# Kernel tuning notes

Hardware: AMD Instinct MI355X
Metric: run time of the kernel (lower is better)

## Reference

```python
import jax, jax.numpy as jnp
import numpy as np

E = 8      # n_rm_states
D = 256    # flattened input dim
H = 64     # hidden width (hard-coded in module)
A = 18     # n_actions
B = 65536  # batch


def setup_inputs() -> dict:
    key = jax.random.key(0)
    ks = jax.random.split(key, 16)
    s = lambda k, shape, fan_in: jax.random.normal(k, shape, jnp.float32) * (1.0 / np.sqrt(fan_in))
    inp = {
        "state": jax.random.normal(ks[0], (B, D), jnp.float32),
        "rm_state": jax.random.randint(ks[1], (B,), 0, E),
        # stacked per-expert params: layer i weight [E, in, out], bias [E, out]
        "W1": s(ks[2], (E, D, H), D), "b1": jnp.zeros((E, H), jnp.float32),
        "W2": s(ks[3], (E, H, H), H), "b2": jnp.zeros((E, H), jnp.float32),
        "W3": s(ks[4], (E, H, H), H), "b3": jnp.zeros((E, H), jnp.float32),
        "W4": s(ks[5], (E, H, H), H), "b4": jnp.zeros((E, H), jnp.float32),
        "W5": s(ks[6], (E, H, H), H), "b5": jnp.zeros((E, H), jnp.float32),
        "W6": s(ks[7], (E, H, A), H), "b6": jnp.zeros((E, A), jnp.float32),
    }
    return inp


def reference(state, rm_state, W1, b1, W2, b2, W3, b3, W4, b4, W5, b5, W6, b6):
    x = state.reshape(state.shape[0], -1)              # [B, D]
    # Run all E expert MLPs densely over the batch, then select per-row expert.
    h = jax.nn.relu(jnp.einsum('bd,edh->ebh', x, W1) + b1[:, None, :])   # [E, B, H]
    h = jax.nn.relu(jnp.einsum('ebh,ehk->ebk', h, W2) + b2[:, None, :])
    h = jax.nn.relu(jnp.einsum('ebh,ehk->ebk', h, W3) + b3[:, None, :])
    h = jax.nn.relu(jnp.einsum('ebh,ehk->ebk', h, W4) + b4[:, None, :])
    h = jax.nn.relu(jnp.einsum('ebh,ehk->ebk', h, W5) + b5[:, None, :])
    out_all = jnp.einsum('ebh,eha->eba', h, W6) + b6[:, None, :]          # [E, B, A]
    # scatter-back: actions[b] = expert[rm_state[b]](x[b])
    actions = out_all[rm_state, jnp.arange(x.shape[0])]                    # [B, A]
    return actions
```

## Files before the change

kernel.cpp:

```cpp
#include <hip/hip_runtime.h>
#include <hip/hip_bf16.h>


#define NE   8
#define DIM  256
#define HID  64
#define NA   18

typedef __attribute__((ext_vector_type(8))) short short8;
typedef __attribute__((ext_vector_type(4))) float f32x4;
#define MFMA __builtin_amdgcn_mfma_f32_16x16x32_bf16

__device__ __forceinline__ unsigned short f2bf(float f) {
    unsigned u = __builtin_bit_cast(unsigned, f);
    u += 0x7fff + ((u >> 16) & 1);
    return (unsigned short)(u >> 16);
}
__device__ __forceinline__ float bf2f(unsigned short h) {
    unsigned u = ((unsigned)h) << 16;
    return __builtin_bit_cast(float, u);
}
__device__ __forceinline__ void split8v(const float* xs, short8& hi, short8& lo) {
    float back[8];
    #pragma unroll
    for (int p = 0; p < 4; ++p) {
        __hip_bfloat162 h2 = __float22bfloat162_rn(make_float2(xs[2*p], xs[2*p+1]));
        hi[2*p]   = (short)__builtin_bit_cast(unsigned short, h2.x);
        hi[2*p+1] = (short)__builtin_bit_cast(unsigned short, h2.y);
        float2 b2 = __bfloat1622float2(h2);
        back[2*p] = b2.x; back[2*p+1] = b2.y;
    }
    #pragma unroll
    for (int p = 0; p < 4; ++p) {
        __hip_bfloat162 l2 = __float22bfloat162_rn(
            make_float2(xs[2*p] - back[2*p], xs[2*p+1] - back[2*p+1]));
        lo[2*p]   = (short)__builtin_bit_cast(unsigned short, l2.x);
        lo[2*p+1] = (short)__builtin_bit_cast(unsigned short, l2.y);
    }
}

__global__ __launch_bounds__(256) void prep_histo(
    const float* __restrict__ W1, const float* __restrict__ W2,
    const float* __restrict__ W3, const float* __restrict__ W4,
    const float* __restrict__ W5, const float* __restrict__ W6,
    short* __restrict__ W1H, short* __restrict__ W1L,
    short* __restrict__ W2H, short* __restrict__ W2L,
    short* __restrict__ W3H, short* __restrict__ W3L,
    short* __restrict__ W4H, short* __restrict__ W4L,
    short* __restrict__ W5H, short* __restrict__ W5L,
    short* __restrict__ W6H, short* __restrict__ W6L,
    const int* __restrict__ rm, int* __restrict__ hist) {
    const int bid = blockIdx.x;
    if (bid >= 136) {
        __shared__ int wch[4][NE];
        const int blk = bid - 136;
        const int t = threadIdx.x, w = t >> 6, l = t & 63;
        const int e = rm[blk * 256 + t];
        #pragma unroll
        for (int q = 0; q < NE; ++q) {
            unsigned long long m = __ballot(e == q);
            if (l == 0) wch[w][q] = __popcll(m);
        }
        __syncthreads();
        if (t < NE) hist[blk * NE + t] = wch[0][t] + wch[1][t] + wch[2][t] + wch[3][t];
        return;
    }
    const int u = bid * 256 + threadIdx.x;
    const float* src; int sstride, dbase, n, npad;
    short *H, *L;
    if (u < 16384) {
        int e = u >> 11, r = u & 2047;
        int ks = r >> 8, nt = (r >> 6) & 3, l = r & 63;
        int k0 = ks * 32 + ((l >> 4) << 3); n = (nt << 4) + (l & 15);
        src = W1 + ((size_t)(e * DIM + k0)) * HID + n;
        sstride = HID; npad = HID;
        H = W1H; L = W1L; dbase = e * 16384 + ((ks * 4 + nt) * 64 + l) * 8;
    } else if (u < 32768) {
        int u2 = u - 16384;
        int layer = u2 >> 12, local = u2 & 4095;
        int e = local >> 9, r = local & 511;
        int ks = r >> 8, nt = (r >> 6) & 3, l = r & 63;
        int k0 = ks * 32 + ((l >> 4) << 3); n = (nt << 4) + (l & 15);
        const float* W = (layer == 0) ? W2 : (layer == 1) ? W3 : (layer == 2) ? W4 : W5;
        src = W + ((size_t)(e * HID + k0)) * HID + n;
        sstride = HID; npad = HID;
        H = (layer == 0) ? W2H : (layer == 1) ? W3H : (layer == 2) ? W4H : W5H;
        L = (layer == 0) ? W2L : (layer == 1) ? W3L : (layer == 2) ? W4L : W5L;
        dbase = e * 4096 + ((ks * 4 + nt) * 64 + l) * 8;
    } else {
        int u3 = u - 32768;
        int e = u3 >> 8, r = u3 & 255;
        int ks = r >> 7, nt = (r >> 6) & 1, l = r & 63;
        int k0 = ks * 32 + ((l >> 4) << 3); n = (nt << 4) + (l & 15);
        src = W6 + ((size_t)(e * HID + k0)) * NA + n;
        sstride = NA; npad = NA;
        H = W6H; L = W6L; dbase = e * 2048 + ((ks * 2 + nt) * 64 + l) * 8;
    }
    short8 hs, ls;
    #pragma unroll
    for (int j = 0; j < 8; ++j) {
        float v = (n < npad) ? src[j * sstride] : 0.0f;
        unsigned short h = f2bf(v);
        hs[j] = (short)h;
        ls[j] = (short)f2bf(v - bf2f(h));
    }
    *(short8*)(H + dbase) = hs;
    *(short8*)(L + dbase) = ls;
}

__global__ __launch_bounds__(512) void scan_scatter(const int* __restrict__ rm,
                                                    const int* __restrict__ hist,
                                                    int* __restrict__ perm,
                                                    int* __restrict__ meta) {
    __shared__ int sbuf[NE][256];
    __shared__ int wc[8][NE];
    __shared__ int wb2[4][NE];
    __shared__ int baseE[NE];
    const int t = threadIdx.x, w = t >> 6, l = t & 63;
    const int myblk = blockIdx.x;

    {
        int v0 = hist[(l * 4 + 0) * NE + w];
        int v1 = hist[(l * 4 + 1) * NE + w];
        int v2 = hist[(l * 4 + 2) * NE + w];
        int v3 = hist[(l * 4 + 3) * NE + w];
        v1 += v0; v2 += v1; v3 += v2;
        int s = v3;
        #pragma unroll
        for (int off = 1; off < 64; off <<= 1) {
            int u = __shfl_up(s, off);
            if (l >= off) s += u;
        }
        const int ex = s - v3;
        sbuf[w][l * 4 + 0] = ex + v0;
        sbuf[w][l * 4 + 1] = ex + v1;
        sbuf[w][l * 4 + 2] = ex + v2;
        sbuf[w][l * 4 + 3] = ex + v3;
    }
    __syncthreads();
    if (t < NE) {
        int es = 0;
        for (int q = 0; q < t; ++q) es += sbuf[q][255];
        baseE[t] = es + (myblk ? sbuf[t][myblk - 1] : 0);
    }
    if (myblk == 0 && t == 0) {
        int es = 0, ts = 0;
        meta[8] = 0; meta[17] = 0;
        for (int e = 0; e < NE; ++e) {
            int c = sbuf[e][255];
            meta[e] = c;
            es += c; meta[8 + e + 1] = es;
            ts += (c + 127) >> 7; meta[17 + e + 1] = ts;
        }
    }
    const int i = myblk * 256 + t;
    const int e_row = (t < 256) ? rm[i] : -1;
    const unsigned long long ltm = (1ull << l) - 1ull;
    int rank = 0;
    #pragma unroll
    for (int q = 0; q < NE; ++q) {
        unsigned long long m = __ballot(e_row == q);
        if (e_row == q) rank = __popcll(m & ltm);
        if (l == 0) wc[w][q] = __popcll(m);
    }
    __syncthreads();
    if (t < 32) {
        int ww = t >> 3, q = t & 7;
        int b = baseE[q];
        for (int p = 0; p < ww; ++p) b += wc[p][q];
        wb2[ww][q] = b;
    }
    __syncthreads();
    if (t < 256) perm[wb2[w][e_row] + rank] = i;
}

template <int NT>
__device__ __forceinline__ void gemm2_k64(const float* h0, const float* h1, int l,
                                          const short* __restrict__ WH,
                                          const short* __restrict__ WL,
                                          f32x4 (*a0)[NT], f32x4 (*a1)[NT],
                                          f32x4 (*a2)[NT]) {
    const int lg = l >> 4, lr = l & 15;
    #pragma unroll
    for (int ks = 0; ks < 2; ++ks) {
        const float* ap0 = h0 + lr * 68 + ks * 32 + lg * 8;
        const float* ap1 = h1 + lr * 68 + ks * 32 + lg * 8;
        float4 u0 = *(const float4*)(ap0);
        float4 u1 = *(const float4*)(ap0 + 4);
        float4 v0 = *(const float4*)(ap1);
        float4 v1 = *(const float4*)(ap1 + 4);
        float xs0[8] = {u0.x, u0.y, u0.z, u0.w, u1.x, u1.y, u1.z, u1.w};
        float xs1[8] = {v0.x, v0.y, v0.z, v0.w, v1.x, v1.y, v1.z, v1.w};
        short8 ahi0, alo0, ahi1, alo1;
        split8v(xs0, ahi0, alo0);
        split8v(xs1, ahi1, alo1);
        short8 bh[NT], bl[NT];
        #pragma unroll
        for (int nt = 0; nt < NT; ++nt) {
            bh[nt] = *(const short8*)(WH + ((ks * NT + nt) * 64 + l) * 8);
            bl[nt] = *(const short8*)(WL + ((ks * NT + nt) * 64 + l) * 8);
        }
        #pragma unroll
        for (int nt = 0; nt < NT; ++nt) {
            a0[0][nt] = MFMA(ahi0, bh[nt], a0[0][nt], 0, 0, 0);
            a0[1][nt] = MFMA(ahi1, bh[nt], a0[1][nt], 0, 0, 0);
            a1[0][nt] = MFMA(alo0, bh[nt], a1[0][nt], 0, 0, 0);
            a1[1][nt] = MFMA(alo1, bh[nt], a1[1][nt], 0, 0, 0);
            a2[0][nt] = MFMA(ahi0, bl[nt], a2[0][nt], 0, 0, 0);
            a2[1][nt] = MFMA(ahi1, bl[nt], a2[1][nt], 0, 0, 0);
        }
    }
}

template <int NT, bool RELU>
__device__ __forceinline__ void finish2(float* h0, float* h1, int l,
                                        const float* __restrict__ bias,
                                        f32x4 (*a0)[NT], f32x4 (*a1)[NT],
                                        f32x4 (*a2)[NT]) {
    const int lg = l >> 4, lr = l & 15;
    #pragma unroll
    for (int nt = 0; nt < NT; ++nt) {
        float bv = bias[nt * 16 + lr];
        #pragma unroll
        for (int r = 0; r < 4; ++r) {
            float v0 = (a0[0][nt][r] + a1[0][nt][r]) + (a2[0][nt][r] + bv);
            float v1 = (a0[1][nt][r] + a1[1][nt][r]) + (a2[1][nt][r] + bv);
            if (RELU) { v0 = fmaxf(v0, 0.0f); v1 = fmaxf(v1, 0.0f); }
            h0[(lg * 4 + r) * 68 + nt * 16 + lr] = v0;
            h1[(lg * 4 + r) * 68 + nt * 16 + lr] = v1;
        }
    }
}

__global__ __launch_bounds__(256, 2) void mlp_mfma(
    const float* __restrict__ x, const int* __restrict__ perm,
    const int* __restrict__ meta,
    const short* __restrict__ W1H, const short* __restrict__ W1L,
    const short* __restrict__ W2H, const short* __restrict__ W2L,
    const short* __restrict__ W3H, const short* __restrict__ W3L,
    const short* __restrict__ W4H, const short* __restrict__ W4L,
    const short* __restrict__ W5H, const short* __restrict__ W5L,
    const short* __restrict__ W6H, const short* __restrict__ W6L,
    const float* __restrict__ b1, const float* __restrict__ b2,
    const float* __restrict__ b3, const float* __restrict__ b4,
    const float* __restrict__ b5, const float* __restrict__ b6,
    float* __restrict__ out) {
    __shared__ __align__(16) float hbuf[4][2][16][68];
    const int blk = blockIdx.x;
    if (blk >= meta[17 + NE]) return;
    int e = 0;
    #pragma unroll 1
    while (blk >= meta[17 + e + 1]) ++e;
    const int lt = blk - meta[17 + e];
    const int cnt = meta[e];
    const int pbase = meta[8 + e];
    const int t = threadIdx.x, w = t >> 6, l = t & 63;
    const int lg = l >> 4, lr = l & 15;
    const int li0 = lt * 128 + w * 32 + lr;
    const int li1 = li0 + 16;
    const int row0 = perm[pbase + min(li0, cnt - 1)];
    const int row1 = perm[pbase + min(li1, cnt - 1)];
    float* h0 = &hbuf[w][0][0][0];
    float* h1 = &hbuf[w][1][0][0];
    const f32x4 zero = {0.0f, 0.0f, 0.0f, 0.0f};

    {
        f32x4 a0[2][4], a1[2][4], a2[2][4];
        #pragma unroll
        for (int m = 0; m < 2; ++m)
            #pragma unroll
            for (int nt = 0; nt < 4; ++nt) { a0[m][nt] = zero; a1[m][nt] = zero; a2[m][nt] = zero; }
        const float* xr0 = x + (size_t)row0 * DIM + lg * 8;
        const float* xr1 = x + (size_t)row1 * DIM + lg * 8;
        const short* WHp = W1H + (size_t)e * 16384 + l * 8;
        const short* WLp = W1L + (size_t)e * 16384 + l * 8;
        #pragma unroll
        for (int ks = 0; ks < 8; ++ks) {
            float4 u0 = *(const float4*)(xr0 + ks * 32);
            float4 u1 = *(const float4*)(xr0 + ks * 32 + 4);
            float4 v0 = *(const float4*)(xr1 + ks * 32);
            float4 v1 = *(const float4*)(xr1 + ks * 32 + 4);
            float xs0[8] = {u0.x, u0.y, u0.z, u0.w, u1.x, u1.y, u1.z, u1.w};
            float xs1[8] = {v0.x, v0.y, v0.z, v0.w, v1.x, v1.y, v1.z, v1.w};
            short8 ahi0, alo0, ahi1, alo1;
            split8v(xs0, ahi0, alo0);
            split8v(xs1, ahi1, alo1);
            short8 bh[4], bl[4];
            #pragma unroll
            for (int nt = 0; nt < 4; ++nt) {
                bh[nt] = *(const short8*)(WHp + (ks * 4 + nt) * 512);
                bl[nt] = *(const short8*)(WLp + (ks * 4 + nt) * 512);
            }
            #pragma unroll
            for (int nt = 0; nt < 4; ++nt) {
                a0[0][nt] = MFMA(ahi0, bh[nt], a0[0][nt], 0, 0, 0);
                a0[1][nt] = MFMA(ahi1, bh[nt], a0[1][nt], 0, 0, 0);
                a1[0][nt] = MFMA(alo0, bh[nt], a1[0][nt], 0, 0, 0);
                a1[1][nt] = MFMA(alo1, bh[nt], a1[1][nt], 0, 0, 0);
                a2[0][nt] = MFMA(ahi0, bl[nt], a2[0][nt], 0, 0, 0);
                a2[1][nt] = MFMA(ahi1, bl[nt], a2[1][nt], 0, 0, 0);
            }
        }
        finish2<4, true>(h0, h1, l, b1 + e * HID, a0, a1, a2);
    }
    #define HIDDEN(WH_, WL_, bias_)                                         \
    {                                                                       \
        f32x4 a0[2][4], a1[2][4], a2[2][4];                                 \
        _Pragma("unroll")                                                   \
        for (int m = 0; m < 2; ++m)                                         \
            _Pragma("unroll")                                               \
            for (int nt = 0; nt < 4; ++nt) { a0[m][nt] = zero; a1[m][nt] = zero; a2[m][nt] = zero; } \
        gemm2_k64<4>(h0, h1, l, WH_ + e * 4096, WL_ + e * 4096, a0, a1, a2);\
        finish2<4, true>(h0, h1, l, bias_ + e * HID, a0, a1, a2);           \
    }
    HIDDEN(W2H, W2L, b2)
    HIDDEN(W3H, W3L, b3)
    HIDDEN(W4H, W4L, b4)
    HIDDEN(W5H, W5L, b5)
    #undef HIDDEN
    {
        f32x4 a0[2][2], a1[2][2], a2[2][2];
        #pragma unroll
        for (int m = 0; m < 2; ++m)
            #pragma unroll
            for (int nt = 0; nt < 2; ++nt) { a0[m][nt] = zero; a1[m][nt] = zero; a2[m][nt] = zero; }
        gemm2_k64<2>(h0, h1, l, W6H + e * 2048, W6L + e * 2048, a0, a1, a2);
        const float* b6p = b6 + e * NA;
        #pragma unroll
        for (int m = 0; m < 2; ++m) {
            const int rowm = m ? row1 : row0;
            #pragma unroll
            for (int r = 0; r < 4; ++r) {
                const int drow = lg * 4 + r;
                const int rs = __shfl(rowm, drow, 64);
                const bool valid = (lt * 128 + w * 32 + m * 16 + drow) < cnt;
                #pragma unroll
                for (int nt = 0; nt < 2; ++nt) {
                    const int col = nt * 16 + lr;
                    if (valid && col < NA)
                        out[(size_t)rs * NA + col] =
                            (a0[m][nt][r] + a1[m][nt][r]) + (a2[m][nt][r] + b6p[col]);
                }
            }
        }
    }
}

extern "C" void kernel_launch(void* const* d_in, const int* in_sizes, int n_in,
                              void* d_out, int out_size, void* d_ws, size_t ws_size,
                              hipStream_t stream) {
    const float* x  = (const float*)d_in[0];
    const int*   rm = (const int*)d_in[1];
    const float* W1 = (const float*)d_in[2];   const float* b1 = (const float*)d_in[3];
    const float* W2 = (const float*)d_in[4];   const float* b2 = (const float*)d_in[5];
    const float* W3 = (const float*)d_in[6];   const float* b3 = (const float*)d_in[7];
    const float* W4 = (const float*)d_in[8];   const float* b4 = (const float*)d_in[9];
    const float* W5 = (const float*)d_in[10];  const float* b5 = (const float*)d_in[11];
    const float* W6 = (const float*)d_in[12];  const float* b6 = (const float*)d_in[13];
    float* out = (float*)d_out;

    const int B = in_sizes[1];
    const int nblk = B / 256;

    int* hist = (int*)d_ws;
    int* meta = hist + nblk * NE;
    int* perm = meta + 32;
    short* W1H = (short*)(perm + B);
    short* W1L = W1H + 131072;
    short* W2H = W1L + 131072;  short* W2L = W2H + 32768;
    short* W3H = W2L + 32768;   short* W3L = W3H + 32768;
    short* W4H = W3L + 32768;   short* W4L = W4H + 32768;
    short* W5H = W4L + 32768;   short* W5L = W5H + 32768;
    short* W6H = W5L + 32768;   short* W6L = W6H + 16384;

    prep_histo<<<136 + nblk, 256, 0, stream>>>(W1, W2, W3, W4, W5, W6,
                                               W1H, W1L, W2H, W2L, W3H, W3L,
                                               W4H, W4L, W5H, W5L, W6H, W6L,
                                               rm, hist);
    scan_scatter<<<nblk, 512, 0, stream>>>(rm, hist, perm, meta);
    mlp_mfma<<<B / 128 + NE, 256, 0, stream>>>(x, perm, meta,
                                               W1H, W1L, W2H, W2L, W3H, W3L,
                                               W4H, W4L, W5H, W5L, W6H, W6L,
                                               b1, b2, b3, b4, b5, b6, out);
}
```

Baseline: 155.2 us.

## Split K across waves with 32-row tiles and shared-memory partial sum reduction

Each block now handles 32 rows instead of 128. Its four waves split the work as 2 row groups times 2 K halves, and each wave writes a partial sum to shared memory. The next layer adds the two partials and applies ReLU while loading them. Launch bounds rise to allow 8 blocks per CU, and the grid is four times larger. The intent is more parallelism and occupancy per expert tile and less padding waste per expert, at the cost of extra __syncthreads per layer, fewer row-tiles to reuse each weight load across, and a serialized scalar epilogue.

```diff
diff --git a/kernel.cpp b/kernel.cpp
--- a/kernel.cpp
+++ b/kernel.cpp
@@ -150,7 +150,7 @@
             int c = sbuf[e][255];
             meta[e] = c;
             es += c; meta[8 + e + 1] = es;
-            ts += (c + 127) >> 7; meta[17 + e + 1] = ts;
+            ts += (c + 31) >> 5; meta[17 + e + 1] = ts;
         }
     }
     const int i = myblk * 256 + t;
@@ -174,65 +174,50 @@
     if (t < 256) perm[wb2[w][e_row] + rank] = i;
 }
 
+__device__ __forceinline__ void read_split(const float* pa, const float* pb, int off,
+                                           short8& hi, short8& lo) {
+    float4 a0 = *(const float4*)(pa + off);
+    float4 a1 = *(const float4*)(pa + off + 4);
+    float4 b0 = *(const float4*)(pb + off);
+    float4 b1 = *(const float4*)(pb + off + 4);
+    float xs[8] = {fmaxf(a0.x + b0.x, 0.0f), fmaxf(a0.y + b0.y, 0.0f),
+                   fmaxf(a0.z + b0.z, 0.0f), fmaxf(a0.w + b0.w, 0.0f),
+                   fmaxf(a1.x + b1.x, 0.0f), fmaxf(a1.y + b1.y, 0.0f),
+                   fmaxf(a1.z + b1.z, 0.0f), fmaxf(a1.w + b1.w, 0.0f)};
+    split8v(xs, hi, lo);
+}
+
 template <int NT>
-__device__ __forceinline__ void gemm2_k64(const float* h0, const float* h1, int l,
-                                          const short* __restrict__ WH,
-                                          const short* __restrict__ WL,
-                                          f32x4 (*a0)[NT], f32x4 (*a1)[NT],
-                                          f32x4 (*a2)[NT]) {
+__device__ __forceinline__ void mfma_slice(const short* __restrict__ WH,
+                                           const short* __restrict__ WL,
+                                           int l, int kh,
+                                           const short8& ahi, const short8& alo,
+                                           f32x4* acc) {
+    #pragma unroll
+    for (int nt = 0; nt < NT; ++nt) {
+        short8 bh = *(const short8*)(WH + (kh * NT + nt) * 512 + l * 8);
+        short8 bl = *(const short8*)(WL + (kh * NT + nt) * 512 + l * 8);
+        acc[nt] = MFMA(ahi, bh, acc[nt], 0, 0, 0);
+        acc[nt] = MFMA(alo, bh, acc[nt], 0, 0, 0);
+        acc[nt] = MFMA(ahi, bl, acc[nt], 0, 0, 0);
+    }
+}
+
+template <int NT>
+__device__ __forceinline__ void write_partial(float* pw, int l,
+                                              const float* __restrict__ bias,
+                                              const f32x4* acc) {
     const int lg = l >> 4, lr = l & 15;
     #pragma unroll
-    for (int ks = 0; ks < 2; ++ks) {
-        const float* ap0 = h0 + lr * 68 + ks * 32 + lg * 8;
-        const float* ap1 = h1 + lr * 68 + ks * 32 + lg * 8;
-        float4 u0 = *(const float4*)(ap0);
-        float4 u1 = *(const float4*)(ap0 + 4);
-        float4 v0 = *(const float4*)(ap1);
-        float4 v1 = *(const float4*)(ap1 + 4);
-        float xs0[8] = {u0.x, u0.y, u0.z, u0.w, u1.x, u1.y, u1.z, u1.w};
-        float xs1[8] = {v0.x, v0.y, v0.z, v0.w, v1.x, v1.y, v1.z, v1.w};
-        short8 ahi0, alo0, ahi1, alo1;
-        split8v(xs0, ahi0, alo0);
-        split8v(xs1, ahi1, alo1);
-        short8 bh[NT], bl[NT];
-        #pragma unroll
-        for (int nt = 0; nt < NT; ++nt) {
-            bh[nt] = *(const short8*)(WH + ((ks * NT + nt) * 64 + l) * 8);
-            bl[nt] = *(const short8*)(WL + ((ks * NT + nt) * 64 + l) * 8);
-        }
-        #pragma unroll
-        for (int nt = 0; nt < NT; ++nt) {
-            a0[0][nt] = MFMA(ahi0, bh[nt], a0[0][nt], 0, 0, 0);
-            a0[1][nt] = MFMA(ahi1, bh[nt], a0[1][nt], 0, 0, 0);
-            a1[0][nt] = MFMA(alo0, bh[nt], a1[0][nt], 0, 0, 0);
-            a1[1][nt] = MFMA(alo1, bh[nt], a1[1][nt], 0, 0, 0);
-            a2[0][nt] = MFMA(ahi0, bl[nt], a2[0][nt], 0, 0, 0);
-            a2[1][nt] = MFMA(ahi1, bl[nt], a2[1][nt], 0, 0, 0);
-        }
-    }
-}
-
-template <int NT, bool RELU>
-__device__ __forceinline__ void finish2(float* h0, float* h1, int l,
-                                        const float* __restrict__ bias,
-                                        f32x4 (*a0)[NT], f32x4 (*a1)[NT],
-                                        f32x4 (*a2)[NT]) {
-    const int lg = l >> 4, lr = l & 15;
-    #pragma unroll
     for (int nt = 0; nt < NT; ++nt) {
-        float bv = bias[nt * 16 + lr];
-        #pragma unroll
-        for (int r = 0; r < 4; ++r) {
-            float v0 = (a0[0][nt][r] + a1[0][nt][r]) + (a2[0][nt][r] + bv);
-            float v1 = (a0[1][nt][r] + a1[1][nt][r]) + (a2[1][nt][r] + bv);
-            if (RELU) { v0 = fmaxf(v0, 0.0f); v1 = fmaxf(v1, 0.0f); }
-            h0[(lg * 4 + r) * 68 + nt * 16 + lr] = v0;
-            h1[(lg * 4 + r) * 68 + nt * 16 + lr] = v1;
-        }
-    }
-}
-
-__global__ __launch_bounds__(256, 2) void mlp_mfma(
+        float bv = bias ? bias[nt * 16 + lr] : 0.0f;
+        #pragma unroll
+        for (int r = 0; r < 4; ++r)
+            pw[(lg * 4 + r) * 68 + nt * 16 + lr] = acc[nt][r] + bv;
+    }
+}
+
+__global__ __launch_bounds__(256, 8) void mlp_mfma(
     const float* __restrict__ x, const int* __restrict__ perm,
     const int* __restrict__ meta,
     const short* __restrict__ W1H, const short* __restrict__ W1L,
@@ -245,7 +230,7 @@
     const float* __restrict__ b3, const float* __restrict__ b4,
     const float* __restrict__ b5, const float* __restrict__ b6,
     float* __restrict__ out) {
-    __shared__ __align__(16) float hbuf[4][2][16][68];
+    __shared__ __align__(16) float hbuf[2][2][16][68];
     const int blk = blockIdx.x;
     if (blk >= meta[17 + NE]) return;
     int e = 0;
@@ -255,93 +240,82 @@
     const int cnt = meta[e];
     const int pbase = meta[8 + e];
     const int t = threadIdx.x, w = t >> 6, l = t & 63;
+    const int m = w >> 1, kh = w & 1;
     const int lg = l >> 4, lr = l & 15;
-    const int li0 = lt * 128 + w * 32 + lr;
-    const int li1 = li0 + 16;
-    const int row0 = perm[pbase + min(li0, cnt - 1)];
-    const int row1 = perm[pbase + min(li1, cnt - 1)];
-    float* h0 = &hbuf[w][0][0][0];
-    float* h1 = &hbuf[w][1][0][0];
+    const int li = lt * 32 + m * 16 + lr;
+    const int row = perm[pbase + min(li, cnt - 1)];
+
+    float* pw = &hbuf[kh][m][0][0];
+    const float* pa = &hbuf[0][m][0][0];
+    const float* pb = &hbuf[1][m][0][0];
+    const int roff = lr * 68 + kh * 32 + lg * 8;
     const f32x4 zero = {0.0f, 0.0f, 0.0f, 0.0f};
 
     {
-        f32x4 a0[2][4], a1[2][4], a2[2][4];
-        #pragma unroll
-        for (int m = 0; m < 2; ++m)
-            #pragma unroll
-            for (int nt = 0; nt < 4; ++nt) { a0[m][nt] = zero; a1[m][nt] = zero; a2[m][nt] = zero; }
-        const float* xr0 = x + (size_t)row0 * DIM + lg * 8;
-        const float* xr1 = x + (size_t)row1 * DIM + lg * 8;
-        const short* WHp = W1H + (size_t)e * 16384 + l * 8;
-        const short* WLp = W1L + (size_t)e * 16384 + l * 8;
-        #pragma unroll
-        for (int ks = 0; ks < 8; ++ks) {
-            float4 u0 = *(const float4*)(xr0 + ks * 32);
-            float4 u1 = *(const float4*)(xr0 + ks * 32 + 4);
-            float4 v0 = *(const float4*)(xr1 + ks * 32);
-            float4 v1 = *(const float4*)(xr1 + ks * 32 + 4);
-            float xs0[8] = {u0.x, u0.y, u0.z, u0.w, u1.x, u1.y, u1.z, u1.w};
-            float xs1[8] = {v0.x, v0.y, v0.z, v0.w, v1.x, v1.y, v1.z, v1.w};
-            short8 ahi0, alo0, ahi1, alo1;
-            split8v(xs0, ahi0, alo0);
-            split8v(xs1, ahi1, alo1);
-            short8 bh[4], bl[4];
+        f32x4 a0[4] = {zero, zero, zero, zero};
+        f32x4 a1[4] = {zero, zero, zero, zero};
+        const float* xr = x + (size_t)row * DIM + kh * 128 + lg * 8;
+        const short* WHp = W1H + (size_t)e * 16384;
+        const short* WLp = W1L + (size_t)e * 16384;
+        #pragma unroll
+        for (int ks = 0; ks < 4; ++ks) {
+            float4 u0 = *(const float4*)(xr + ks * 32);
+            float4 u1 = *(const float4*)(xr + ks * 32 + 4);
+            float xs[8] = {u0.x, u0.y, u0.z, u0.w, u1.x, u1.y, u1.z, u1.w};
+            short8 ahi, alo; split8v(xs, ahi, alo);
+            const int ksg = kh * 4 + ks;
             #pragma unroll
             for (int nt = 0; nt < 4; ++nt) {
-                bh[nt] = *(const short8*)(WHp + (ks * 4 + nt) * 512);
-                bl[nt] = *(const short8*)(WLp + (ks * 4 + nt) * 512);
+                short8 bh = *(const short8*)(WHp + (ksg * 4 + nt) * 512 + l * 8);
+                short8 bl = *(const short8*)(WLp + (ksg * 4 + nt) * 512 + l * 8);
+                a0[nt] = MFMA(ahi, bh, a0[nt], 0, 0, 0);
+                a1[nt] = MFMA(alo, bh, a1[nt], 0, 0, 0);
+                a1[nt] = MFMA(ahi, bl, a1[nt], 0, 0, 0);
             }
-            #pragma unroll
-            for (int nt = 0; nt < 4; ++nt) {
-                a0[0][nt] = MFMA(ahi0, bh[nt], a0[0][nt], 0, 0, 0);
-                a0[1][nt] = MFMA(ahi1, bh[nt], a0[1][nt], 0, 0, 0);
-                a1[0][nt] = MFMA(alo0, bh[nt], a1[0][nt], 0, 0, 0);
-                a1[1][nt] = MFMA(alo1, bh[nt], a1[1][nt], 0, 0, 0);
-                a2[0][nt] = MFMA(ahi0, bl[nt], a2[0][nt], 0, 0, 0);
-                a2[1][nt] = MFMA(ahi1, bl[nt], a2[1][nt], 0, 0, 0);
-            }
-        }
-        finish2<4, true>(h0, h1, l, b1 + e * HID, a0, a1, a2);
-    }
-    #define HIDDEN(WH_, WL_, bias_)                                         \
-    {                                                                       \
-        f32x4 a0[2][4], a1[2][4], a2[2][4];                                 \
-        _Pragma("unroll")                                                   \
-        for (int m = 0; m < 2; ++m)                                         \
-            _Pragma("unroll")                                               \
-            for (int nt = 0; nt < 4; ++nt) { a0[m][nt] = zero; a1[m][nt] = zero; a2[m][nt] = zero; } \
-        gemm2_k64<4>(h0, h1, l, WH_ + e * 4096, WL_ + e * 4096, a0, a1, a2);\
-        finish2<4, true>(h0, h1, l, bias_ + e * HID, a0, a1, a2);           \
+        }
+        f32x4 acc[4];
+        #pragma unroll
+        for (int nt = 0; nt < 4; ++nt) acc[nt] = a0[nt] + a1[nt];
+        write_partial<4>(pw, l, (kh == 0) ? b1 + e * HID : nullptr, acc);
+    }
+    __syncthreads();
+
+    #define HIDDEN(WH_, WL_, bias_)                                          \
+    {                                                                        \
+        short8 ahi, alo;                                                     \
+        read_split(pa, pb, roff, ahi, alo);                                  \
+        __syncthreads();                    \
+        f32x4 acc[4] = {zero, zero, zero, zero};                             \
+        mfma_slice<4>(WH_ + e * 4096, WL_ + e * 4096, l, kh, ahi, alo, acc); \
+        write_partial<4>(pw, l, (kh == 0) ? bias_ + e * HID : nullptr, acc); \
+        __syncthreads();                   \
     }
     HIDDEN(W2H, W2L, b2)
     HIDDEN(W3H, W3L, b3)
     HIDDEN(W4H, W4L, b4)
     HIDDEN(W5H, W5L, b5)
     #undef HIDDEN
+
     {
-        f32x4 a0[2][2], a1[2][2], a2[2][2];
-        #pragma unroll
-        for (int m = 0; m < 2; ++m)
-            #pragma unroll
-            for (int nt = 0; nt < 2; ++nt) { a0[m][nt] = zero; a1[m][nt] = zero; a2[m][nt] = zero; }
-        gemm2_k64<2>(h0, h1, l, W6H + e * 2048, W6L + e * 2048, a0, a1, a2);
-        const float* b6p = b6 + e * NA;
-        #pragma unroll
-        for (int m = 0; m < 2; ++m) {
-            const int rowm = m ? row1 : row0;
-            #pragma unroll
-            for (int r = 0; r < 4; ++r) {
-                const int drow = lg * 4 + r;
-                const int rs = __shfl(rowm, drow, 64);
-                const bool valid = (lt * 128 + w * 32 + m * 16 + drow) < cnt;
-                #pragma unroll
-                for (int nt = 0; nt < 2; ++nt) {
-                    const int col = nt * 16 + lr;
-                    if (valid && col < NA)
-                        out[(size_t)rs * NA + col] =
-                            (a0[m][nt][r] + a1[m][nt][r]) + (a2[m][nt][r] + b6p[col]);
-                }
-            }
+        short8 ahi, alo;
+        read_split(pa, pb, roff, ahi, alo);
+        __syncthreads();
+        f32x4 acc[2] = {zero, zero};
+        mfma_slice<2>(W6H + e * 2048, W6L + e * 2048, l, kh, ahi, alo, acc);
+        write_partial<2>(pw, l, nullptr, acc);
+        __syncthreads();
+    }
+    const float* b6p = b6 + e * NA;
+    #pragma unroll
+    for (int idx = t; idx < 2 * 16 * NA; idx += 256) {
+        const int m2 = idx / (16 * NA);
+        const int rr = (idx % (16 * NA)) / NA;
+        const int c  = idx % NA;
+        const int gr = lt * 32 + m2 * 16 + rr;
+        if (gr < cnt) {
+            const int rowid = perm[pbase + gr];
+            out[(size_t)rowid * NA + c] =
+                hbuf[0][m2][rr][c] + hbuf[1][m2][rr][c] + b6p[c];
         }
     }
 }
@@ -378,8 +352,8 @@
                                                W4H, W4L, W5H, W5L, W6H, W6L,
                                                rm, hist);
     scan_scatter<<<nblk, 512, 0, stream>>>(rm, hist, perm, meta);
-    mlp_mfma<<<B / 128 + NE, 256, 0, stream>>>(x, perm, meta,
-                                               W1H, W1L, W2H, W2L, W3H, W3L,
-                                               W4H, W4L, W5H, W5L, W6H, W6L,
-                                               b1, b2, b3, b4, b5, b6, out);
-}
+    mlp_mfma<<<B / 32 + NE, 256, 0, stream>>>(x, perm, meta,
+                                              W1H, W1L, W2H, W2L, W3H, W3L,
+                                              W4H, W4L, W5H, W5L, W6H, W6L,
+                                              b1, b2, b3, b4, b5, b6, out);
+}
```

Measured after the change: 153.1 us. Within noise of the previous version (-1.3%).
